# Kernel optimization log

Measured on AMD Instinct MI355X. Metric: run time of the kernel, lower is better.

The kernel has to match this reference:

```python
import jax, jax.numpy as jnp
import numpy as np

EPS = 1e-5

def binarize(x):
    # sign binarization with straight-through estimator (matches .data replacement in torch BNN code)
    s = jnp.where(x >= 0, 1.0, -1.0).astype(x.dtype)
    return x + jax.lax.stop_gradient(s - x)

def conv3x3(x, w):
    return jax.lax.conv_general_dilated(x, w, (1, 1), ((1, 1), (1, 1)),
                                        dimension_numbers=('NCHW', 'OIHW', 'NCHW'))

def bn4(x, g, b, m, v):
    inv = jax.lax.rsqrt(v + EPS)
    return (x - m[None, :, None, None]) * (g * inv)[None, :, None, None] + b[None, :, None, None]

def bn2(x, g, b, m, v):
    return (x - m) * (g * jax.lax.rsqrt(v + EPS)) + b

def maxpool2(x):
    return jax.lax.reduce_window(x, -jnp.inf, jax.lax.max, (1, 1, 2, 2), (1, 1, 2, 2), 'VALID')

def ht(x):
    return jnp.clip(x, -1.0, 1.0)


def setup_inputs() -> dict:
    key = jax.random.key(0)
    ks = iter(jax.random.split(key, 64))
    d = {}
    d['x'] = jax.random.normal(next(ks), (256, 3, 32, 32), jnp.float32)
    conv_shapes = [(128, 3), (128, 128), (256, 128), (256, 256), (512, 256), (512, 512)]
    for i, (co, ci) in enumerate(conv_shapes, start=1):
        d[f'w{i}'] = jax.random.normal(next(ks), (co, ci, 3, 3), jnp.float32) * 0.05
        d[f'g{i}'] = jax.random.uniform(next(ks), (co,), jnp.float32, 0.5, 1.5)
        d[f'b{i}'] = jax.random.normal(next(ks), (co,), jnp.float32) * 0.1
        d[f'm{i}'] = jax.random.normal(next(ks), (co,), jnp.float32) * 0.1
        d[f'v{i}'] = jax.random.uniform(next(ks), (co,), jnp.float32, 0.5, 1.5)
    d['bias2'] = jax.random.normal(next(ks), (128,), jnp.float32) * 0.1  # conv2 has default bias=True
    fc_shapes = [(1024, 512 * 4 * 4), (1024, 1024), (10, 1024)]
    for j, (co, ci) in enumerate(fc_shapes, start=7):
        d[f'w{j}'] = jax.random.normal(next(ks), (co, ci), jnp.float32) * 0.02
        d[f'm{j}'] = jax.random.normal(next(ks), (co,), jnp.float32) * 0.1
        d[f'v{j}'] = jax.random.uniform(next(ks), (co,), jnp.float32, 0.5, 1.5)
        if j < 9:  # last BN is affine=False
            d[f'g{j}'] = jax.random.uniform(next(ks), (co,), jnp.float32, 0.5, 1.5)
            d[f'b{j}'] = jax.random.normal(next(ks), (co,), jnp.float32) * 0.1
    return d


def reference(x, w1, g1, b1, m1, v1, w2, bias2, g2, b2, m2, v2, w3, g3, b3, m3, v3,
              w4, g4, b4, m4, v4, w5, g5, b5, m5, v5, w6, g6, b6, m6, v6,
              w7, g7, b7, m7, v7, w8, g8, b8, m8, v8, w9, m9, v9):
    # features
    h = conv3x3(x, binarize(w1))                      # first layer: input NOT binarized (3 channels)
    h = ht(bn4(h, g1, b1, m1, v1))
    h = conv3x3(binarize(h), binarize(w2)) + bias2[None, :, None, None]
    h = ht(bn4(maxpool2(h), g2, b2, m2, v2))
    h = conv3x3(binarize(h), binarize(w3))
    h = ht(bn4(h, g3, b3, m3, v3))
    h = conv3x3(binarize(h), binarize(w4))
    h = ht(bn4(maxpool2(h), g4, b4, m4, v4))
    h = conv3x3(binarize(h), binarize(w5))
    h = ht(bn4(h, g5, b5, m5, v5))
    h = conv3x3(binarize(h), binarize(w6))
    h = ht(bn4(maxpool2(h), g6, b6, m6, v6))          # [B, 512, 4, 4]
    # classifier
    h = h.reshape(-1, 512 * 4 * 4)
    h = ht(bn2(binarize(h) @ binarize(w7).T, g7, b7, m7, v7))
    h = ht(bn2(binarize(h) @ binarize(w8).T, g8, b8, m8, v8))
    h = binarize(h) @ binarize(w9).T
    h = (h - m9) * jax.lax.rsqrt(v9 + EPS)            # BatchNorm1d(affine=False)
    return jax.nn.log_softmax(h, axis=-1)
```

## Files before the change

kernel.cpp:

```cpp
#include <hip/hip_runtime.h>
#include <stdint.h>

typedef unsigned long long u64;

static __device__ __forceinline__ int uread(int v) { return __builtin_amdgcn_readfirstlane(v); }
static __device__ __forceinline__ float fr(float x) { __asm__ volatile("" : "+v"(x)); return x; }

static __device__ __forceinline__ bool bn_neg(float x, float g, float b, float m, float v) {
    float inv = fr(1.0f / fr(sqrtf(fr(v + 1e-5f))));
    float si  = fr(g * inv);
    float t1  = fr(x - m);
    float t2  = fr(t1 * si);
    float bn  = fr(t2 + b);
    return bn < 0.0f;
}


__global__ __launch_bounds__(256) void packw1_kernel(const float* __restrict__ w, float* __restrict__ ws) {
    int id = blockIdx.x * 256 + threadIdx.x;
    if (id >= 27 * 128) return;
    int co = id & 127, j = id >> 7;
    ws[j * 128 + co] = (w[co * 27 + j] < 0.f) ? -1.f : 1.f;
}

__global__ __launch_bounds__(256) void packw_conv2_kernel(const float* __restrict__ w, u64* __restrict__ wb,
                                                          int CINW, int COUT) {
    int wv = blockIdx.x * 4 + (threadIdx.x >> 6);
    if (wv >= COUT * CINW) return;
    int lane = threadIdx.x & 63;
    int wrd = wv % CINW, co = wv / CINW;
    int CIN = CINW * 64;
    const float* p = w + ((size_t)co * CIN + (size_t)wrd * 64 + lane) * 9;
    float f[9];
#pragma unroll
    for (int t = 0; t < 9; ++t) f[t] = p[t];
#pragma unroll
    for (int t = 0; t < 9; ++t) {
        u64 bits = __ballot(f[t] < 0.f);
        if (lane == 0) wb[(size_t)(t * CINW + wrd) * COUT + co] = bits;
    }
}

__global__ __launch_bounds__(256) void packw7_kernel(const float* __restrict__ w, u64* __restrict__ wb) {
    int wv = blockIdx.x * 4 + (threadIdx.x >> 6);
    if (wv >= 1024 * 8) return;
    int lane = threadIdx.x & 63;
    int cw = wv & 7, o = wv >> 3;
    const float* p = w + (size_t)o * 8192 + (size_t)(cw * 64 + lane) * 16;
    float f[16];
#pragma unroll
    for (int i = 0; i < 16; i += 4) {
        float4 q = *(const float4*)(p + i);
        f[i] = q.x; f[i + 1] = q.y; f[i + 2] = q.z; f[i + 3] = q.w;
    }
#pragma unroll
    for (int pixel = 0; pixel < 16; ++pixel) {
        u64 bits = __ballot(f[pixel] < 0.f);
        if (lane == 0) wb[(size_t)(pixel * 8 + cw) * 1024 + o] = bits;
    }
}

__global__ __launch_bounds__(256) void packw8_kernel(const float* __restrict__ w, u64* __restrict__ wb) {
    int wv = blockIdx.x * 4 + (threadIdx.x >> 6);
    if (wv >= 1024 * 16) return;
    int lane = threadIdx.x & 63;
    int k = wv & 15, o = wv >> 4;
    float f = w[(size_t)o * 1024 + k * 64 + lane];
    u64 bits = __ballot(f < 0.f);
    if (lane == 0) wb[(size_t)k * 1024 + o] = bits;
}

__global__ __launch_bounds__(256) void packw9_kernel(const float* __restrict__ w, u64* __restrict__ wb) {
    int wv = blockIdx.x * 4 + (threadIdx.x >> 6);
    if (wv >= 160) return;
    int lane = threadIdx.x & 63;
    int k = wv & 15, o = wv >> 4;
    float f = w[(size_t)o * 1024 + k * 64 + lane];
    u64 bits = __ballot(f < 0.f);
    if (lane == 0) wb[k * 16 + o] = bits;
}

__global__ __launch_bounds__(256, 4) void conv1_kernel(
    const float* __restrict__ x, const float* __restrict__ w1s,
    const float* __restrict__ g, const float* __restrict__ bb,
    const float* __restrict__ m, const float* __restrict__ v,
    u64* __restrict__ out, int N)
{
    int lane = threadIdx.x & 63;
    int rid = uread(blockIdx.x * 4 + (threadIdx.x >> 6));
    if (rid >= N * 32) return;
    int n = rid >> 5, y = rid & 31;
    const float* xb = x + (size_t)n * 3072;
    const bool rv0 = (y > 0), rv2 = (y < 31);
    const int y0 = rv0 ? y - 1 : 0, y2 = rv2 ? y + 1 : 31;

    int co0 = lane, co1 = 64 + lane;
    float w0[27], w1[27];
#pragma unroll
    for (int j = 0; j < 27; ++j) {
        w0[j] = fr(w1s[j * 128 + co0]);
        w1[j] = fr(w1s[j * 128 + co1]);
    }
    float g0 = g[co0], b0 = bb[co0], m0 = m[co0], v0 = v[co0];
    float g1 = g[co1], b1 = bb[co1], m1 = m[co1], v1 = v[co1];

    float cm[9], cc[9], cn[9];
#pragma unroll
    for (int t = 0; t < 9; ++t) cm[t] = 0.f;

    auto ldcol = [&](float* c, int xs) {
#pragma unroll
        for (int ci = 0; ci < 3; ++ci) {
            float a0 = xb[ci * 1024 + y0 * 32 + xs];
            float a1 = xb[ci * 1024 + y  * 32 + xs];
            float a2 = xb[ci * 1024 + y2 * 32 + xs];
            c[0 + ci] = fr(rv0 ? a0 : 0.f);
            c[3 + ci] = fr(a1);
            c[6 + ci] = fr(rv2 ? a2 : 0.f);
        }
    };
    ldcol(cc, 0);

    u64* orow = out + (((size_t)n * 32 + y) * 32) * 2;

    for (int xx = 0; xx < 32; ++xx) {
        if (xx < 31) ldcol(cn, xx + 1);
        else {
#pragma unroll
            for (int t = 0; t < 9; ++t) cn[t] = 0.f;
        }
        float a0 = 0.f, a1 = 0.f;
#pragma unroll
        for (int ky = 0; ky < 3; ++ky) {
#pragma unroll
            for (int ci = 0; ci < 3; ++ci) a0 = fmaf(w0[ci * 9 + ky * 3 + 0], cm[ky * 3 + ci], a0);
#pragma unroll
            for (int ci = 0; ci < 3; ++ci) a0 = fmaf(w0[ci * 9 + ky * 3 + 1], cc[ky * 3 + ci], a0);
#pragma unroll
            for (int ci = 0; ci < 3; ++ci) a0 = fmaf(w0[ci * 9 + ky * 3 + 2], cn[ky * 3 + ci], a0);
        }
#pragma unroll
        for (int ky = 0; ky < 3; ++ky) {
#pragma unroll
            for (int ci = 0; ci < 3; ++ci) a1 = fmaf(w1[ci * 9 + ky * 3 + 0], cm[ky * 3 + ci], a1);
#pragma unroll
            for (int ci = 0; ci < 3; ++ci) a1 = fmaf(w1[ci * 9 + ky * 3 + 1], cc[ky * 3 + ci], a1);
#pragma unroll
            for (int ci = 0; ci < 3; ++ci) a1 = fmaf(w1[ci * 9 + ky * 3 + 2], cn[ky * 3 + ci], a1);
        }
        u64 bits0 = __ballot(bn_neg(a0, g0, b0, m0, v0));
        u64 bits1 = __ballot(bn_neg(a1, g1, b1, m1, v1));
        if (lane == 0) {
            ulonglong2 st; st.x = bits0; st.y = bits1;
            *(ulonglong2*)(orow + xx * 2) = st;
        }
#pragma unroll
        for (int t = 0; t < 9; ++t) { cm[t] = cc[t]; cc[t] = cn[t]; }
    }
}

template<int WORDS, int COW, bool POOL, bool HAS_BIAS, int H, int YS, int MINW>
__global__ __launch_bounds__(256, MINW) void binconv_lds(
    const u64* __restrict__ a, const u64* __restrict__ wb,
    const float* __restrict__ g, const float* __restrict__ bb,
    const float* __restrict__ m, const float* __restrict__ v,
    const float* __restrict__ bias, u64* __restrict__ out, int N)
{
    const int W = H;
    const int OH = POOL ? H / 2 : H, OW = POOL ? W / 2 : W;
    const int COUT = COW * 64;
    const int OROWS = OH / YS;
    const int RMAX = POOL ? OROWS * 2 + 2 : OROWS + 2;
    const int PR = POOL ? 4 : 3;
    const int NW = POOL ? 4 : 1;
    const int W2 = WORDS / 2;
    const int S = POOL ? 2 : 1;
    const int NBC = 9 * WORDS * 64;
    const int GPX = (OW <= 4) ? OW : ((NW == 4) ? 4 : OW);
    const int NG = OW / GPX;

    __shared__ alignas(16) u64 tile[RMAX * W * WORDS];

    int blk = blockIdx.x;
    int ys = blk % YS, n = blk / YS;
    int oy0 = ys * OROWS;
    int iy0 = (POOL ? oy0 * 2 - 1 : oy0 - 1); if (iy0 < 0) iy0 = 0;
    int iy1 = (POOL ? (oy0 + OROWS - 1) * 2 + 2 : oy0 + OROWS); if (iy1 > H - 1) iy1 = H - 1;
    int R = iy1 - iy0 + 1;
    {
        const u64* src = a + ((size_t)(n * H + iy0) * W) * WORDS;
        int tot = R * W * WORDS;
        for (int i = threadIdx.x; i < tot; i += 256) tile[i] = src[i];
    }
    __syncthreads();

    int lane = threadIdx.x & 63;
    int wv = uread((int)(threadIdx.x >> 6));

    int cw0, r0, r1;
    if (COW >= 4) { cw0 = wv; r0 = 0; r1 = OROWS; }
    else { cw0 = wv % COW; int chunk = OROWS * COW / 4; r0 = (wv / COW) * chunk; r1 = r0 + chunk; }

    const ulonglong2* t2 = (const ulonglong2*)tile;

    for (int cw = cw0; cw < COW; cw += 4) {
        int co = cw * 64 + lane;
        float gc = g[co], bc = bb[co], mc = m[co], vc = v[co];
        float bi = HAS_BIAS ? bias[co] : 0.f;

        auto store_px = [&](int oy, int ox, int best) {
            float tv = (float)best;
            if (HAS_BIAS) tv = fr(tv + bi);
            u64 bits = __ballot(bn_neg(tv, gc, bc, mc, vc));
            if (lane == 0) out[((size_t)(n * OH + oy) * OW + ox) * COW + cw] = bits;
        };

        if constexpr (W2 == 1) {
            u64 wgt[18];
#pragma unroll
            for (int t = 0; t < 18; ++t) wgt[t] = wb[(size_t)t * COUT + co];

            auto px_general = [&](int oy, int ox) {
                int y0 = (POOL ? oy * 2 : oy) - 1;
                bool rv[PR];
#pragma unroll
                for (int p = 0; p < PR; ++p) rv[p] = ((unsigned)(y0 + p) < (unsigned)H);
                int x0 = (POOL ? ox * 2 : ox) - 1;
                bool cv[PR];
#pragma unroll
                for (int q = 0; q < PR; ++q) cv[q] = ((unsigned)(x0 + q) < (unsigned)W);

                int acc[NW], nb[NW];
#pragma unroll
                for (int i = 0; i < NW; ++i) { acc[i] = 0; nb[i] = 0; }
#pragma unroll
                for (int sy = 0; sy < (POOL ? 2 : 1); ++sy)
#pragma unroll
                for (int sx = 0; sx < (POOL ? 2 : 1); ++sx)
#pragma unroll
                for (int ky = 0; ky < 3; ++ky)
#pragma unroll
                for (int kx = 0; kx < 3; ++kx)
                    if (rv[sy + ky] && cv[sx + kx]) nb[POOL ? sy * 2 + sx : 0] += WORDS * 64;

                ulonglong2 pt[PR][PR];
#pragma unroll
                for (int p = 0; p < PR; ++p) if (rv[p]) {
                    int lrow = y0 + p - iy0;
#pragma unroll
                    for (int q = 0; q < PR; ++q) if (cv[q])
                        pt[p][q] = t2[(lrow * W + (x0 + q))];
                }
#pragma unroll
                for (int sy = 0; sy < (POOL ? 2 : 1); ++sy)
#pragma unroll
                for (int sx = 0; sx < (POOL ? 2 : 1); ++sx)
#pragma unroll
                for (int ky = 0; ky < 3; ++ky)
#pragma unroll
                for (int kx = 0; kx < 3; ++kx)
                    if (rv[sy + ky] && cv[sx + kx]) {
                        ulonglong2 q = pt[sy + ky][sx + kx];
                        int wi = POOL ? sy * 2 + sx : 0;
                        acc[wi] += __popcll(q.x ^ wgt[(ky * 3 + kx) * 2])
                                 + __popcll(q.y ^ wgt[(ky * 3 + kx) * 2 + 1]);
                    }
                int best = 0;
#pragma unroll
                for (int i = 0; i < NW; ++i) {
                    int dot = nb[i] - 2 * acc[i];
                    best = (i == 0) ? dot : max(best, dot);
                }
                store_px(oy, ox, best);
            };

            for (int oy = oy0 + r0; oy < oy0 + r1; ++oy) {
                int y0 = (POOL ? oy * 2 : oy) - 1;
                if (y0 < 0 || y0 + PR > H) {
                    for (int ox = 0; ox < OW; ++ox) px_general(oy, ox);
                    continue;
                }
                int base = y0 - iy0;
                px_general(oy, 0);
                ulonglong2 win[PR][PR];
                const int xl = POOL ? 1 : 0;
#pragma unroll
                for (int p = 0; p < PR; ++p)
#pragma unroll
                    for (int q = 0; q < PR; ++q)
                        win[p][q] = t2[(base + p) * W + xl + q];
                for (int ox = 1; ox < OW - 1; ++ox) {
                    int acc[NW];
#pragma unroll
                    for (int i = 0; i < NW; ++i) acc[i] = 0;
#pragma unroll
                    for (int sy = 0; sy < (POOL ? 2 : 1); ++sy)
#pragma unroll
                    for (int sx = 0; sx < (POOL ? 2 : 1); ++sx)
#pragma unroll
                    for (int ky = 0; ky < 3; ++ky)
#pragma unroll
                    for (int kx = 0; kx < 3; ++kx) {
                        ulonglong2 q = win[sy + ky][sx + kx];
                        int wi = POOL ? sy * 2 + sx : 0;
                        acc[wi] += __popcll(q.x ^ wgt[(ky * 3 + kx) * 2])
                                 + __popcll(q.y ^ wgt[(ky * 3 + kx) * 2 + 1]);
                    }
                    int best = 0;
#pragma unroll
                    for (int i = 0; i < NW; ++i) {
                        int dot = NBC - 2 * acc[i];
                        best = (i == 0) ? dot : max(best, dot);
                    }
                    store_px(oy, ox, best);
                    if (ox < OW - 2) {
                        int xnew = (POOL ? ox * 2 - 1 : ox - 1) + PR;
#pragma unroll
                        for (int p = 0; p < PR; ++p) {
#pragma unroll
                            for (int q = 0; q < PR - S; ++q) win[p][q] = win[p][q + S];
#pragma unroll
                            for (int s = 0; s < S; ++s)
                                win[p][PR - S + s] = t2[(base + p) * W + xnew + s];
                        }
                    }
                }
                px_general(oy, OW - 1);
            }
        } else {
            for (int oy = oy0 + r0; oy < oy0 + r1; ++oy) {
                int y0r = (POOL ? oy * 2 : oy) - 1;
                bool rv[PR];
#pragma unroll
                for (int p = 0; p < PR; ++p) rv[p] = ((unsigned)(y0r + p) < (unsigned)H);
                int baseR = y0r - iy0;

#pragma unroll
                for (int gg = 0; gg < NG; ++gg) {
                    int acc[GPX][NW];
#pragma unroll
                    for (int i = 0; i < GPX; ++i)
#pragma unroll
                        for (int wi = 0; wi < NW; ++wi) acc[i][wi] = 0;

#pragma unroll 1
                    for (int w2 = 0; w2 < W2; ++w2) {
                        u64 wc[18];
#pragma unroll
                        for (int t = 0; t < 9; ++t) {
                            wc[t * 2]     = wb[(size_t)(t * WORDS + 2 * w2) * COUT + co];
                            wc[t * 2 + 1] = wb[(size_t)(t * WORDS + 2 * w2 + 1) * COUT + co];
                        }
                        ulonglong2 win[PR][PR];
#pragma unroll
                        for (int i = 0; i < GPX; ++i) {
                            const int ox = gg * GPX + i;
                            const int x0 = S * ox - 1;
                            if (i == 0) {
#pragma unroll
                                for (int q = 0; q < PR; ++q) {
                                    const int x = x0 + q;
                                    if (x >= 0 && x < W) {
#pragma unroll
                                        for (int p = 0; p < PR; ++p)
                                            if (rv[p]) win[p][q] = t2[((baseR + p) * W + x) * W2 + w2];
                                    }
                                }
                            } else {
#pragma unroll
                                for (int p = 0; p < PR; ++p)
#pragma unroll
                                    for (int q = 0; q < PR - S; ++q) win[p][q] = win[p][q + S];
#pragma unroll
                                for (int s = 0; s < S; ++s) {
                                    const int x = x0 + PR - S + s;
                                    if (x >= 0 && x < W) {
#pragma unroll
                                        for (int p = 0; p < PR; ++p)
                                            if (rv[p]) win[p][PR - S + s] = t2[((baseR + p) * W + x) * W2 + w2];
                                    }
                                }
                            }
#pragma unroll
                            for (int sy = 0; sy < (POOL ? 2 : 1); ++sy)
#pragma unroll
                            for (int sx = 0; sx < (POOL ? 2 : 1); ++sx)
#pragma unroll
                            for (int ky = 0; ky < 3; ++ky)
#pragma unroll
                            for (int kx = 0; kx < 3; ++kx) {
                                const int xq = x0 + sx + kx;
                                if (xq >= 0 && xq < W) {
                                    if (rv[sy + ky]) {
                                        ulonglong2 q = win[sy + ky][sx + kx];
                                        const int t = ky * 3 + kx;
                                        const int wi = POOL ? sy * 2 + sx : 0;
                                        acc[i][wi] += __popcll(q.x ^ wc[t * 2])
                                                    + __popcll(q.y ^ wc[t * 2 + 1]);
                                    }
                                }
                            }
                        }
                    }

#pragma unroll
                    for (int i = 0; i < GPX; ++i) {
                        const int ox = gg * GPX + i;
                        const int x0 = S * ox - 1;
                        int nb[NW];
#pragma unroll
                        for (int wi = 0; wi < NW; ++wi) nb[wi] = 0;
#pragma unroll
                        for (int sy = 0; sy < (POOL ? 2 : 1); ++sy)
#pragma unroll
                        for (int sx = 0; sx < (POOL ? 2 : 1); ++sx)
#pragma unroll
                        for (int ky = 0; ky < 3; ++ky)
#pragma unroll
                        for (int kx = 0; kx < 3; ++kx) {
                            const int xq = x0 + sx + kx;
                            if (xq >= 0 && xq < W) {
                                if (rv[sy + ky]) nb[POOL ? sy * 2 + sx : 0] += WORDS * 64;
                            }
                        }
                        int best = 0;
#pragma unroll
                        for (int wi = 0; wi < NW; ++wi) {
                            int dot = nb[wi] - 2 * acc[i][wi];
                            best = (wi == 0) ? dot : max(best, dot);
                        }
                        store_px(oy, ox, best);
                    }
                }
            }
        }
    }
}

template<int KW, int OWRD>
__global__ __launch_bounds__(256) void binfc_kernel(
    const u64* __restrict__ a, const u64* __restrict__ wb,
    const float* __restrict__ g, const float* __restrict__ bb,
    const float* __restrict__ m, const float* __restrict__ v,
    u64* __restrict__ out, int N)
{
    int lane = threadIdx.x & 63;
    int wid = uread(blockIdx.x * 4 + (threadIdx.x >> 6));
    if (wid >= N * OWRD) return;
    int ow = wid & (OWRD - 1), n = wid / OWRD;
    int o = ow * 64 + lane;
    const u64* ap = a + (size_t)n * KW;
    int acc = 0;
#pragma unroll 8
    for (int k = 0; k < KW; ++k)
        acc += __popcll(ap[k] ^ wb[(size_t)k * (OWRD * 64) + o]);
    float dotf = (float)(KW * 64 - 2 * acc);
    u64 bits = __ballot(bn_neg(dotf, g[o], bb[o], m[o], v[o]));
    if (lane == 0) out[(size_t)n * OWRD + ow] = bits;
}

__global__ __launch_bounds__(64) void fc9_kernel(
    const u64* __restrict__ a, const u64* __restrict__ wb,
    const float* __restrict__ m, const float* __restrict__ v, float* __restrict__ out)
{
    int n = blockIdx.x, t = threadIdx.x;
    const u64* ap = a + (size_t)n * 16;
    float val = -1e30f;
    if (t < 10) {
        int acc = 0;
#pragma unroll
        for (int k = 0; k < 16; ++k) acc += __popcll(ap[k] ^ wb[k * 16 + t]);
        float dotf = (float)(1024 - 2 * acc);
        float inv = fr(1.0f / fr(sqrtf(fr(v[t] + 1e-5f))));
        float t1  = fr(dotf - m[t]);
        val = fr(t1 * inv);
    }
    float mx = val;
#pragma unroll
    for (int off = 32; off; off >>= 1) mx = fmaxf(mx, __shfl_xor(mx, off));
    float sh = fr(val - mx);
    double e = (t < 10) ? exp((double)sh) : 0.0;
    double sum = e;
#pragma unroll
    for (int off = 32; off; off >>= 1) sum += __shfl_xor(sum, off);
    if (t < 10) out[n * 10 + t] = (float)((double)sh - log(sum));
}

extern "C" void kernel_launch(void* const* d_in, const int* in_sizes, int n_in,
                              void* d_out, int out_size, void* d_ws, size_t ws_size,
                              hipStream_t stream) {
    auto F = [&](int i) { return (const float*)d_in[i]; };
    const float* x  = F(0);
    const float* w1 = F(1);  const float* g1 = F(2);  const float* b1 = F(3);
    const float* m1 = F(4);  const float* v1 = F(5);
    const float* w2 = F(6);  const float* g2 = F(7);  const float* b2 = F(8);
    const float* m2 = F(9);  const float* v2 = F(10);
    const float* w3 = F(11); const float* g3 = F(12); const float* b3 = F(13);
    const float* m3 = F(14); const float* v3 = F(15);
    const float* w4 = F(16); const float* g4 = F(17); const float* b4 = F(18);
    const float* m4 = F(19); const float* v4 = F(20);
    const float* w5 = F(21); const float* g5 = F(22); const float* b5 = F(23);
    const float* m5 = F(24); const float* v5 = F(25);
    const float* w6 = F(26); const float* g6 = F(27); const float* b6 = F(28);
    const float* m6 = F(29); const float* v6 = F(30);
    const float* bias2 = F(31);
    const float* w7 = F(32); const float* m7 = F(33); const float* v7 = F(34);
    const float* g7 = F(35); const float* b7 = F(36);
    const float* w8 = F(37); const float* m8 = F(38); const float* v8 = F(39);
    const float* g8 = F(40); const float* b8 = F(41);
    const float* w9 = F(42); const float* m9 = F(43); const float* v9 = F(44);
    (void)in_sizes; (void)n_in; (void)ws_size;

    const int N = out_size / 10;
    u64* ws = (u64*)d_ws;
    size_t off = 0;
    auto carve = [&](size_t nwords) { u64* p = ws + off; off += nwords; return p; };
    float* w1s = (float*)carve(1728);
    u64* w2p = carve(2304);
    u64* w3p = carve(4608);
    u64* w4p = carve(9216);
    u64* w5p = carve(18432);
    u64* w6p = carve(36864);
    u64* w7p = carve(131072);
    u64* w8p = carve(16384);
    u64* w9p = carve(256);
    u64* a1 = carve((size_t)N * 32 * 32 * 2);
    u64* a2 = carve((size_t)N * 16 * 16 * 2);
    u64* a3 = carve((size_t)N * 16 * 16 * 4);
    u64* a4 = carve((size_t)N * 8 * 8 * 4);
    u64* a5 = carve((size_t)N * 8 * 8 * 8);
    u64* a6 = carve((size_t)N * 16 * 8);
    u64* f7 = carve((size_t)N * 16);
    u64* f8 = carve((size_t)N * 16);

    packw1_kernel<<<(3456 + 255) / 256, 256, 0, stream>>>(w1, w1s);
    packw_conv2_kernel<<<(128 * 2 + 3) / 4, 256, 0, stream>>>(w2, w2p, 2, 128);
    packw_conv2_kernel<<<(256 * 2 + 3) / 4, 256, 0, stream>>>(w3, w3p, 2, 256);
    packw_conv2_kernel<<<(256 * 4 + 3) / 4, 256, 0, stream>>>(w4, w4p, 4, 256);
    packw_conv2_kernel<<<(512 * 4 + 3) / 4, 256, 0, stream>>>(w5, w5p, 4, 512);
    packw_conv2_kernel<<<(512 * 8 + 3) / 4, 256, 0, stream>>>(w6, w6p, 8, 512);
    packw7_kernel<<<(8192 + 3) / 4, 256, 0, stream>>>(w7, w7p);
    packw8_kernel<<<(16384 + 3) / 4, 256, 0, stream>>>(w8, w8p);
    packw9_kernel<<<(160 + 3) / 4, 256, 0, stream>>>(w9, w9p);

    conv1_kernel<<<(N * 32 + 3) / 4, 256, 0, stream>>>(x, w1s, g1, b1, m1, v1, a1, N);

    binconv_lds<2, 2, true, true, 32, 4, 3><<<N * 4, 256, 0, stream>>>(
        a1, w2p, g2, b2, m2, v2, bias2, a2, N);
    binconv_lds<2, 4, false, false, 16, 4, 3><<<N * 4, 256, 0, stream>>>(
        a2, w3p, g3, b3, m3, v3, nullptr, a3, N);
    binconv_lds<4, 4, true, false, 16, 4, 3><<<N * 4, 256, 0, stream>>>(
        a3, w4p, g4, b4, m4, v4, nullptr, a4, N);
    binconv_lds<4, 8, false, false, 8, 4, 4><<<N * 4, 256, 0, stream>>>(
        a4, w5p, g5, b5, m5, v5, nullptr, a5, N);
    binconv_lds<8, 8, true, false, 8, 4, 4><<<N * 4, 256, 0, stream>>>(
        a5, w6p, g6, b6, m6, v6, nullptr, a6, N);

    binfc_kernel<128, 16><<<(N * 16 + 3) / 4, 256, 0, stream>>>(a6, w7p, g7, b7, m7, v7, f7, N);
    binfc_kernel<16, 16><<<(N * 16 + 3) / 4, 256, 0, stream>>>(f7, w8p, g8, b8, m8, v8, f8, N);

    fc9_kernel<<<N, 64, 0, stream>>>(f8, w9p, m9, v9, (float*)d_out);
}
```

Before: 680.3 us.

## Fuse weight packing, precompute BN scale, retune conv grids and window loads

```diff
diff --git a/kernel.cpp b/kernel.cpp
--- a/kernel.cpp
+++ b/kernel.cpp
@@ -6,28 +6,25 @@
 static __device__ __forceinline__ int uread(int v) { return __builtin_amdgcn_readfirstlane(v); }
 static __device__ __forceinline__ float fr(float x) { __asm__ volatile("" : "+v"(x)); return x; }
 
-static __device__ __forceinline__ bool bn_neg(float x, float g, float b, float m, float v) {
-    float inv = fr(1.0f / fr(sqrtf(fr(v + 1e-5f))));
-    float si  = fr(g * inv);
-    float t1  = fr(x - m);
-    float t2  = fr(t1 * si);
-    float bn  = fr(t2 + b);
+static __device__ __forceinline__ float bn_scale(float g, float v) {
+    return fr(g * fr(1.0f / fr(sqrtf(fr(v + 1e-5f)))));
+}
+static __device__ __forceinline__ bool bn_neg_s(float x, float si, float b, float m) {
+    float t1 = fr(x - m);
+    float t2 = fr(t1 * si);
+    float bn = fr(t2 + b);
     return bn < 0.0f;
 }
 
 
-__global__ __launch_bounds__(256) void packw1_kernel(const float* __restrict__ w, float* __restrict__ ws) {
-    int id = blockIdx.x * 256 + threadIdx.x;
+__device__ __forceinline__ void d_packw1(const float* __restrict__ w, float* __restrict__ ws, int id) {
     if (id >= 27 * 128) return;
     int co = id & 127, j = id >> 7;
     ws[j * 128 + co] = (w[co * 27 + j] < 0.f) ? -1.f : 1.f;
 }
 
-__global__ __launch_bounds__(256) void packw_conv2_kernel(const float* __restrict__ w, u64* __restrict__ wb,
-                                                          int CINW, int COUT) {
-    int wv = blockIdx.x * 4 + (threadIdx.x >> 6);
-    if (wv >= COUT * CINW) return;
-    int lane = threadIdx.x & 63;
+__device__ __forceinline__ void d_pack_conv(const float* __restrict__ w, u64* __restrict__ wb,
+                                            int CINW, int COUT, int wv, int lane) {
     int wrd = wv % CINW, co = wv / CINW;
     int CIN = CINW * 64;
     const float* p = w + ((size_t)co * CIN + (size_t)wrd * 64 + lane) * 9;
@@ -41,10 +38,7 @@
     }
 }
 
-__global__ __launch_bounds__(256) void packw7_kernel(const float* __restrict__ w, u64* __restrict__ wb) {
-    int wv = blockIdx.x * 4 + (threadIdx.x >> 6);
-    if (wv >= 1024 * 8) return;
-    int lane = threadIdx.x & 63;
+__device__ __forceinline__ void d_packw7(const float* __restrict__ w, u64* __restrict__ wb, int wv, int lane) {
     int cw = wv & 7, o = wv >> 3;
     const float* p = w + (size_t)o * 8192 + (size_t)(cw * 64 + lane) * 16;
     float f[16];
@@ -60,24 +54,44 @@
     }
 }
 
-__global__ __launch_bounds__(256) void packw8_kernel(const float* __restrict__ w, u64* __restrict__ wb) {
-    int wv = blockIdx.x * 4 + (threadIdx.x >> 6);
-    if (wv >= 1024 * 16) return;
-    int lane = threadIdx.x & 63;
+__device__ __forceinline__ void d_packw8(const float* __restrict__ w, u64* __restrict__ wb, int wv, int lane) {
     int k = wv & 15, o = wv >> 4;
     float f = w[(size_t)o * 1024 + k * 64 + lane];
     u64 bits = __ballot(f < 0.f);
     if (lane == 0) wb[(size_t)k * 1024 + o] = bits;
 }
 
-__global__ __launch_bounds__(256) void packw9_kernel(const float* __restrict__ w, u64* __restrict__ wb) {
-    int wv = blockIdx.x * 4 + (threadIdx.x >> 6);
+__device__ __forceinline__ void d_packw9(const float* __restrict__ w, u64* __restrict__ wb, int wv, int lane) {
     if (wv >= 160) return;
-    int lane = threadIdx.x & 63;
     int k = wv & 15, o = wv >> 4;
     float f = w[(size_t)o * 1024 + k * 64 + lane];
     u64 bits = __ballot(f < 0.f);
     if (lane == 0) wb[k * 16 + o] = bits;
+}
+
+__global__ __launch_bounds__(256) void pack_all_kernel(
+    const float* __restrict__ w1, float* __restrict__ w1s,
+    const float* __restrict__ w2, u64* __restrict__ w2p,
+    const float* __restrict__ w3, u64* __restrict__ w3p,
+    const float* __restrict__ w4, u64* __restrict__ w4p,
+    const float* __restrict__ w5, u64* __restrict__ w5p,
+    const float* __restrict__ w6, u64* __restrict__ w6p,
+    const float* __restrict__ w7, u64* __restrict__ w7p,
+    const float* __restrict__ w8, u64* __restrict__ w8p,
+    const float* __restrict__ w9, u64* __restrict__ w9p)
+{
+    int b = blockIdx.x;
+    int lane = threadIdx.x & 63;
+    int wq = threadIdx.x >> 6;
+    if (b < 14) { d_packw1(w1, w1s, b * 256 + threadIdx.x); return; } b -= 14;
+    if (b < 64) { d_pack_conv(w2, w2p, 2, 128, b * 4 + wq, lane); return; } b -= 64;
+    if (b < 128) { d_pack_conv(w3, w3p, 2, 256, b * 4 + wq, lane); return; } b -= 128;
+    if (b < 256) { d_pack_conv(w4, w4p, 4, 256, b * 4 + wq, lane); return; } b -= 256;
+    if (b < 512) { d_pack_conv(w5, w5p, 4, 512, b * 4 + wq, lane); return; } b -= 512;
+    if (b < 1024) { d_pack_conv(w6, w6p, 8, 512, b * 4 + wq, lane); return; } b -= 1024;
+    if (b < 2048) { d_packw7(w7, w7p, b * 4 + wq, lane); return; } b -= 2048;
+    if (b < 4096) { d_packw8(w8, w8p, b * 4 + wq, lane); return; } b -= 4096;
+    d_packw9(w9, w9p, b * 4 + wq, lane);
 }
 
 __global__ __launch_bounds__(256, 4) void conv1_kernel(
@@ -101,8 +115,10 @@
         w0[j] = fr(w1s[j * 128 + co0]);
         w1[j] = fr(w1s[j * 128 + co1]);
     }
-    float g0 = g[co0], b0 = bb[co0], m0 = m[co0], v0 = v[co0];
-    float g1 = g[co1], b1 = bb[co1], m1 = m[co1], v1 = v[co1];
+    float b0 = bb[co0], m0 = m[co0];
+    float b1 = bb[co1], m1 = m[co1];
+    float si0 = bn_scale(g[co0], v[co0]);
+    float si1 = bn_scale(g[co1], v[co1]);
 
     float cm[9], cc[9], cn[9];
 #pragma unroll
@@ -148,8 +164,8 @@
 #pragma unroll
             for (int ci = 0; ci < 3; ++ci) a1 = fmaf(w1[ci * 9 + ky * 3 + 2], cn[ky * 3 + ci], a1);
         }
-        u64 bits0 = __ballot(bn_neg(a0, g0, b0, m0, v0));
-        u64 bits1 = __ballot(bn_neg(a1, g1, b1, m1, v1));
+        u64 bits0 = __ballot(bn_neg_s(a0, si0, b0, m0));
+        u64 bits1 = __ballot(bn_neg_s(a1, si1, b1, m1));
         if (lane == 0) {
             ulonglong2 st; st.x = bits0; st.y = bits1;
             *(ulonglong2*)(orow + xx * 2) = st;
@@ -159,8 +175,8 @@
     }
 }
 
-template<int WORDS, int COW, bool POOL, bool HAS_BIAS, int H, int YS, int MINW>
-__global__ __launch_bounds__(256, MINW) void binconv_lds(
+template<int WORDS, int COW, bool POOL, bool HAS_BIAS, int H, int YS, int NWAVES, int MINW>
+__global__ __launch_bounds__(NWAVES * 64, MINW) void binconv_lds(
     const u64* __restrict__ a, const u64* __restrict__ wb,
     const float* __restrict__ g, const float* __restrict__ bb,
     const float* __restrict__ m, const float* __restrict__ v,
@@ -190,7 +206,7 @@
     {
         const u64* src = a + ((size_t)(n * H + iy0) * W) * WORDS;
         int tot = R * W * WORDS;
-        for (int i = threadIdx.x; i < tot; i += 256) tile[i] = src[i];
+        for (int i = threadIdx.x; i < tot; i += NWAVES * 64) tile[i] = src[i];
     }
     __syncthreads();
 
@@ -198,20 +214,21 @@
     int wv = uread((int)(threadIdx.x >> 6));
 
     int cw0, r0, r1;
-    if (COW >= 4) { cw0 = wv; r0 = 0; r1 = OROWS; }
-    else { cw0 = wv % COW; int chunk = OROWS * COW / 4; r0 = (wv / COW) * chunk; r1 = r0 + chunk; }
+    if (COW >= NWAVES) { cw0 = wv; r0 = 0; r1 = OROWS; }
+    else { cw0 = wv % COW; int chunk = OROWS * COW / NWAVES; r0 = (wv / COW) * chunk; r1 = r0 + chunk; }
 
     const ulonglong2* t2 = (const ulonglong2*)tile;
 
-    for (int cw = cw0; cw < COW; cw += 4) {
+    for (int cw = cw0; cw < COW; cw += NWAVES) {
         int co = cw * 64 + lane;
-        float gc = g[co], bc = bb[co], mc = m[co], vc = v[co];
+        float bc = bb[co], mc = m[co];
+        float sic = bn_scale(g[co], v[co]);
         float bi = HAS_BIAS ? bias[co] : 0.f;
 
         auto store_px = [&](int oy, int ox, int best) {
             float tv = (float)best;
             if (HAS_BIAS) tv = fr(tv + bi);
-            u64 bits = __ballot(bn_neg(tv, gc, bc, mc, vc));
+            u64 bits = __ballot(bn_neg_s(tv, sic, bc, mc));
             if (lane == 0) out[((size_t)(n * OH + oy) * OW + ox) * COW + cw] = bits;
         };
 
@@ -282,17 +299,18 @@
                 }
                 int base = y0 - iy0;
                 px_general(oy, 0);
-                ulonglong2 win[PR][PR];
-                const int xl = POOL ? 1 : 0;
-#pragma unroll
-                for (int p = 0; p < PR; ++p)
-#pragma unroll
-                    for (int q = 0; q < PR; ++q)
-                        win[p][q] = t2[(base + p) * W + xl + q];
                 for (int ox = 1; ox < OW - 1; ++ox) {
+                    int x0 = S * ox - 1;
                     int acc[NW];
 #pragma unroll
                     for (int i = 0; i < NW; ++i) acc[i] = 0;
+                    ulonglong2 win[PR][PR];
+#pragma unroll
+                    for (int p = 0; p < PR; ++p) {
+                        const ulonglong2* rp = t2 + (base + p) * W + x0;
+#pragma unroll
+                        for (int q = 0; q < PR; ++q) win[p][q] = rp[q];
+                    }
 #pragma unroll
                     for (int sy = 0; sy < (POOL ? 2 : 1); ++sy)
 #pragma unroll
@@ -313,17 +331,6 @@
                         best = (i == 0) ? dot : max(best, dot);
                     }
                     store_px(oy, ox, best);
-                    if (ox < OW - 2) {
-                        int xnew = (POOL ? ox * 2 - 1 : ox - 1) + PR;
-#pragma unroll
-                        for (int p = 0; p < PR; ++p) {
-#pragma unroll
-                            for (int q = 0; q < PR - S; ++q) win[p][q] = win[p][q + S];
-#pragma unroll
-                            for (int s = 0; s < S; ++s)
-                                win[p][PR - S + s] = t2[(base + p) * W + xnew + s];
-                        }
-                    }
                 }
                 px_general(oy, OW - 1);
             }
@@ -455,7 +462,8 @@
     for (int k = 0; k < KW; ++k)
         acc += __popcll(ap[k] ^ wb[(size_t)k * (OWRD * 64) + o]);
     float dotf = (float)(KW * 64 - 2 * acc);
-    u64 bits = __ballot(bn_neg(dotf, g[o], bb[o], m[o], v[o]));
+    float si = bn_scale(g[o], v[o]);
+    u64 bits = __ballot(bn_neg_s(dotf, si, bb[o], m[o]));
     if (lane == 0) out[(size_t)n * OWRD + ow] = bits;
 }
 
@@ -533,27 +541,20 @@
     u64* f7 = carve((size_t)N * 16);
     u64* f8 = carve((size_t)N * 16);
 
-    packw1_kernel<<<(3456 + 255) / 256, 256, 0, stream>>>(w1, w1s);
-    packw_conv2_kernel<<<(128 * 2 + 3) / 4, 256, 0, stream>>>(w2, w2p, 2, 128);
-    packw_conv2_kernel<<<(256 * 2 + 3) / 4, 256, 0, stream>>>(w3, w3p, 2, 256);
-    packw_conv2_kernel<<<(256 * 4 + 3) / 4, 256, 0, stream>>>(w4, w4p, 4, 256);
-    packw_conv2_kernel<<<(512 * 4 + 3) / 4, 256, 0, stream>>>(w5, w5p, 4, 512);
-    packw_conv2_kernel<<<(512 * 8 + 3) / 4, 256, 0, stream>>>(w6, w6p, 8, 512);
-    packw7_kernel<<<(8192 + 3) / 4, 256, 0, stream>>>(w7, w7p);
-    packw8_kernel<<<(16384 + 3) / 4, 256, 0, stream>>>(w8, w8p);
-    packw9_kernel<<<(160 + 3) / 4, 256, 0, stream>>>(w9, w9p);
+    pack_all_kernel<<<8182, 256, 0, stream>>>(w1, w1s, w2, w2p, w3, w3p, w4, w4p,
+                                              w5, w5p, w6, w6p, w7, w7p, w8, w8p, w9, w9p);
 
     conv1_kernel<<<(N * 32 + 3) / 4, 256, 0, stream>>>(x, w1s, g1, b1, m1, v1, a1, N);
 
-    binconv_lds<2, 2, true, true, 32, 4, 3><<<N * 4, 256, 0, stream>>>(
+    binconv_lds<2, 2, true, true, 32, 8, 4, 8><<<N * 8, 256, 0, stream>>>(
         a1, w2p, g2, b2, m2, v2, bias2, a2, N);
-    binconv_lds<2, 4, false, false, 16, 4, 3><<<N * 4, 256, 0, stream>>>(
+    binconv_lds<2, 4, false, false, 16, 8, 4, 8><<<N * 8, 256, 0, stream>>>(
         a2, w3p, g3, b3, m3, v3, nullptr, a3, N);
-    binconv_lds<4, 4, true, false, 16, 4, 3><<<N * 4, 256, 0, stream>>>(
+    binconv_lds<4, 4, true, false, 16, 8, 4, 4><<<N * 8, 256, 0, stream>>>(
         a3, w4p, g4, b4, m4, v4, nullptr, a4, N);
-    binconv_lds<4, 8, false, false, 8, 4, 4><<<N * 4, 256, 0, stream>>>(
+    binconv_lds<4, 8, false, false, 8, 8, 4, 4><<<N * 8, 256, 0, stream>>>(
         a4, w5p, g5, b5, m5, v5, nullptr, a5, N);
-    binconv_lds<8, 8, true, false, 8, 4, 4><<<N * 4, 256, 0, stream>>>(
+    binconv_lds<8, 8, true, false, 8, 4, 8, 6><<<N * 4, 512, 0, stream>>>(
         a5, w6p, g6, b6, m6, v6, nullptr, a6, N);
 
     binfc_kernel<128, 16><<<(N * 16 + 3) / 4, 256, 0, stream>>>(a6, w7p, g7, b7, m7, v7, f7, N);
```

Result: slower. 1.721 ms (+153.0%).
